# Performance work log

Hardware: AMD Instinct MI355X
Metric: run time of the kernel (lower is better)

## Reference

```python
import jax, jax.numpy as jnp
import numpy as np


def setup_inputs() -> dict:
    key = jax.random.key(0)
    k1, k2, k3, k4 = jax.random.split(key, 4)
    B, D = 16384, 512
    return {
        "p_mu": jax.random.normal(k1, (B, D), dtype=jnp.float32),
        "p_log_var": jax.random.normal(k2, (B, D), dtype=jnp.float32),
        "q_mu": jax.random.normal(k3, (B, D), dtype=jnp.float32),
        "q_log_var": jax.random.normal(k4, (B, D), dtype=jnp.float32),
    }


def reference(p_mu, p_log_var, q_mu, q_log_var):
    # KL(p || q) for diagonal Gaussians (closed form of the MultivariateNormal KL
    # the torch module computes via diag_embed + Cholesky):
    # 0.5 * sum_d [ log(q_var/p_var) + p_var/q_var + (p_mu-q_mu)^2/q_var - 1 ]
    log_ratio = q_log_var - p_log_var
    kl = 0.5 * jnp.sum(
        log_ratio
        + jnp.exp(-log_ratio)  # p_var / q_var
        + (p_mu - q_mu) ** 2 * jnp.exp(-q_log_var)
        - 1.0,
        axis=-1,
    )
    return jnp.mean(kl)
```

## Files before the change

### kernel.cpp

```cpp
#include <hip/hip_runtime.h>


typedef float vf4 __attribute__((ext_vector_type(4)));

__device__ __forceinline__ float kl4(const vf4 a, const vf4 b,
                                     const vf4 c, const vf4 d) {
  float acc = 0.0f, lr, dx;
  #pragma unroll
  for (int k = 0; k < 4; ++k) {
    lr = d[k] - b[k];
    dx = a[k] - c[k];
    acc += lr + __expf(-lr) + dx * dx * __expf(-d[k]) - 1.0f;
  }
  return acc;
}

__device__ __forceinline__ float block_reduce_256(float acc) {
  #pragma unroll
  for (int off = 32; off > 0; off >>= 1)
    acc += __shfl_down(acc, off, 64);
  __shared__ float sm[4];
  const int lane = threadIdx.x & 63;
  const int wid  = threadIdx.x >> 6;
  if (lane == 0) sm[wid] = acc;
  __syncthreads();
  return sm[0] + sm[1] + sm[2] + sm[3];
}

__global__ __launch_bounds__(256) void kl_partial_kernel(
    const vf4* __restrict__ pmu,
    const vf4* __restrict__ plv,
    const vf4* __restrict__ qmu,
    const vf4* __restrict__ qlv,
    float* __restrict__ partials) {
  const int base = blockIdx.x * 1024 + threadIdx.x;

  vf4 A[4], Bv[4], C[4], Dv[4];
  #pragma unroll
  for (int t = 0; t < 4; ++t) {
    const int i = base + t * 256;
    A[t]  = __builtin_nontemporal_load(&pmu[i]);
    Bv[t] = __builtin_nontemporal_load(&plv[i]);
    C[t]  = __builtin_nontemporal_load(&qmu[i]);
    Dv[t] = __builtin_nontemporal_load(&qlv[i]);
  }

  float acc = 0.0f;
  #pragma unroll
  for (int t = 0; t < 4; ++t)
    acc += kl4(A[t], Bv[t], C[t], Dv[t]);

  const float blocksum = block_reduce_256(acc);
  if (threadIdx.x == 0) partials[blockIdx.x] = blocksum;
}

__global__ __launch_bounds__(256) void kl_final_kernel(
    const float* __restrict__ partials, float* __restrict__ out,
    int nparts, float scale) {
  float acc = 0.0f;
  for (int i = threadIdx.x; i < nparts; i += 256) acc += partials[i];
  const float total = block_reduce_256(acc);
  if (threadIdx.x == 0) out[0] = total * scale;
}

extern "C" void kernel_launch(void* const* d_in, const int* in_sizes, int n_in,
                              void* d_out, int out_size, void* d_ws, size_t ws_size,
                              hipStream_t stream) {
  const vf4* pmu = (const vf4*)d_in[0];
  const vf4* plv = (const vf4*)d_in[1];
  const vf4* qmu = (const vf4*)d_in[2];
  const vf4* qlv = (const vf4*)d_in[3];
  float* out = (float*)d_out;
  float* partials = (float*)d_ws;

  const int B = 16384;
  const float scale = 0.5f / (float)B;

  const int block = 256;
  const int grid = 2048;
  kl_partial_kernel<<<grid, block, 0, stream>>>(pmu, plv, qmu, qlv, partials);
  kl_final_kernel<<<1, block, 0, stream>>>(partials, out, grid, scale);
}
```

Baseline: 142.6 us.

## Stage inputs through LDS with direct global-to-LDS loads and double grid

Replaces register nontemporal vector loads with global_load_lds direct-to-LDS transfers of all four arrays into a 32KB shared buffer, then computes from LDS after a barrier. Each block now handles half as much data and the grid is doubled. Intended to bypass VGPR staging and increase memory-level parallelism, at the cost of LDS occupancy limits, an extra barrier, and loss of the nontemporal hint.

Result: slower. 149.2 us (+4.6%).

```diff
diff --git a/kernel.cpp b/kernel.cpp
--- a/kernel.cpp
+++ b/kernel.cpp
@@ -27,31 +27,46 @@
   return sm[0] + sm[1] + sm[2] + sm[3];
 }
 
+__device__ __forceinline__ void load_to_lds16(const vf4* g, vf4* l) {
+  __builtin_amdgcn_global_load_lds(
+      (const __attribute__((address_space(1))) void*)g,
+      (__attribute__((address_space(3))) void*)l, 16, 0, 0);
+}
+
 __global__ __launch_bounds__(256) void kl_partial_kernel(
     const vf4* __restrict__ pmu,
     const vf4* __restrict__ plv,
     const vf4* __restrict__ qmu,
     const vf4* __restrict__ qlv,
     float* __restrict__ partials) {
-  const int base = blockIdx.x * 1024 + threadIdx.x;
+  __shared__ vf4 lds[4 * 512];
 
-  vf4 A[4], Bv[4], C[4], Dv[4];
+  const int tid  = threadIdx.x;
+  const int lane = tid & 63;
+  const int w    = tid >> 6;
+  const int gbase = blockIdx.x * 512;
+
+  const vf4* arrs[4] = {pmu, plv, qmu, qlv};
   #pragma unroll
-  for (int t = 0; t < 4; ++t) {
-    const int i = base + t * 256;
-    A[t]  = __builtin_nontemporal_load(&pmu[i]);
-    Bv[t] = __builtin_nontemporal_load(&plv[i]);
-    C[t]  = __builtin_nontemporal_load(&qmu[i]);
-    Dv[t] = __builtin_nontemporal_load(&qlv[i]);
+  for (int arr = 0; arr < 4; ++arr) {
+    #pragma unroll
+    for (int t = 0; t < 2; ++t) {
+      const int off = w * 128 + t * 64;
+      load_to_lds16(&arrs[arr][gbase + off + lane], &lds[arr * 512 + off]);
+    }
   }
+  __syncthreads();
 
   float acc = 0.0f;
   #pragma unroll
-  for (int t = 0; t < 4; ++t)
-    acc += kl4(A[t], Bv[t], C[t], Dv[t]);
+  for (int k = 0; k < 2; ++k) {
+    const int idx = tid + k * 256;
+    acc += kl4(lds[0 * 512 + idx], lds[1 * 512 + idx],
+               lds[2 * 512 + idx], lds[3 * 512 + idx]);
+  }
 
   const float blocksum = block_reduce_256(acc);
-  if (threadIdx.x == 0) partials[blockIdx.x] = blocksum;
+  if (tid == 0) partials[blockIdx.x] = blocksum;
 }
 
 __global__ __launch_bounds__(256) void kl_final_kernel(
@@ -77,7 +92,7 @@
   const float scale = 0.5f / (float)B;
 
   const int block = 256;
-  const int grid = 2048;
+  const int grid = 4096;
   kl_partial_kernel<<<grid, block, 0, stream>>>(pmu, plv, qmu, qlv, partials);
   kl_final_kernel<<<1, block, 0, stream>>>(partials, out, grid, scale);
 }
```
